# Kernel tuning notes

Hardware: AMD Instinct MI355X
Metric: run time of the kernel (lower is better)

## Reference

```python
import jax, jax.numpy as jnp
import numpy as np

NUM_HEADS = 12
LEVEL = 16
SOFTMAX_STEP = 6.0  # spiking_softmax.step

def _if_init(shape):
    # torch lazily inits q = zeros + 0.5, acc_q = zeros
    return (jnp.full(shape, 0.5, jnp.float32), jnp.zeros(shape, jnp.float32))

def _if_step(state, x, pos_max, neg_min):
    # IFNeuron with q_threshold = 1.0, borrow = 0.0 (all t-branches collapse to q += x.detach())
    q, acc = state
    q = q + jax.lax.stop_gradient(x)
    acc = jnp.round(acc)
    pos = (q - 1.0 >= 0.0) & (acc < pos_max)
    neg = (q < 0.0) & (acc > neg_min)
    out = jnp.where(pos, 1.0, jnp.where(neg, -1.0, 0.0)).astype(jnp.float32)
    return (q - out, acc + out), out

def _forward(x, w_qkv, w_proj):
    T, B, N, C = x.shape
    H = NUM_HEADS
    D = C // H
    scale = D ** -0.5
    pos_s, neg_s = LEVEL // 2 - 1, -(LEVEL // 2)  # sym=True IF neurons
    pos_u, neg_u = LEVEL // 2 - 1, 0              # sym=False (attn_softmax_IF)

    carry = (
        _if_init((B, H, N, D)), _if_init((B, H, N, D)), _if_init((B, H, N, D)),  # q/k/v IF
        _if_init((B, H, N, N)), _if_init((B, H, N, N)),                           # attn IF, softmax IF
        _if_init((B, H, N, D)), _if_init((B, N, C)),                              # after-attn IF, proj IF
        jnp.zeros((B, H, N, N), jnp.float32), jnp.zeros((B, H, N, N), jnp.float32),  # Ssoftmax X, Y_pre
    )

    def step(carry, xs):
        xt, t = xs
        qif, kif, vif, aif, sif, oif, pif, sm_X, sm_Y = carry
        qkv = (xt @ w_qkv.T).reshape(B, N, 3, H, D).transpose(2, 0, 3, 1, 4)  # [3,B,H,N,D]
        qif, q = _if_step(qif, qkv[0], pos_s, neg_s)
        kif, k = _if_step(kif, qkv[1], pos_s, neg_s)
        vif, v = _if_step(vif, qkv[2], pos_s, neg_s)
        q_s = q * scale
        q_acc = qif[1] * scale  # acc_q * scale * q_threshold (thr=1)
        k_acc = kif[1]
        # AttentionMulti incremental-sum QK^T: q_sum@k^T + q@k_sum^T - q@k^T
        attn = (jnp.einsum('bhnd,bhmd->bhnm', q_acc, k)
                + jnp.einsum('bhnd,bhmd->bhnm', q_s, k_acc)
                - jnp.einsum('bhnd,bhmd->bhnm', q_s, k))
        aif, attn = _if_step(aif, attn, pos_s, neg_s)
        # spiking_softmax: delta of (scaled) softmax over accumulated logits
        sm_X = sm_X + attn
        Y = jax.nn.softmax(sm_X, axis=-1) * jnp.minimum(t / SOFTMAX_STEP, 1.0)
        attn = Y - sm_Y
        sm_Y = Y
        sif, attn = _if_step(sif, attn, pos_u, neg_u)
        # AttentionMulti1 incremental-sum attn@V: a_sum@v + a@v_sum - a@v
        out = (jnp.einsum('bhnm,bhmd->bhnd', sif[1], v)
               + jnp.einsum('bhnm,bhmd->bhnd', attn, vif[1])
               - jnp.einsum('bhnm,bhmd->bhnd', attn, v))
        oif, out = _if_step(oif, out, pos_s, neg_s)
        out = out.transpose(0, 2, 1, 3).reshape(B, N, C) @ w_proj.T
        pif, out = _if_step(pif, out, pos_s, neg_s)
        return (qif, kif, vif, aif, sif, oif, pif, sm_X, sm_Y), out

    ts = jnp.arange(1, T + 1, dtype=jnp.float32)
    _, ys = jax.lax.scan(step, carry, (x, ts))
    return ys  # [T, B, N, C] spike outputs per timestep

def setup_inputs():
    key = jax.random.key(0)
    k1, k2, k3 = jax.random.split(key, 3)
    T, B, N, C = 8, 8, 512, 768
    x = jax.random.normal(k1, (T, B, N, C), jnp.float32)
    w_qkv = jax.random.normal(k2, (3 * C, C), jnp.float32) / np.sqrt(C)
    w_proj = jax.random.normal(k3, (C, C), jnp.float32) / np.sqrt(C)
    return {"x": x, "w_qkv": w_qkv, "w_proj": w_proj}

def reference(x, w_qkv, w_proj):
    return _forward(x, w_qkv, w_proj)
```

## Files before the change

### kernel.cpp

```cpp
#include <hip/hip_runtime.h>
#include <stdint.h>

typedef __attribute__((ext_vector_type(4))) float f32x4;
typedef __attribute__((ext_vector_type(8))) short s16x8;
typedef __attribute__((ext_vector_type(8))) char  s8x8;
typedef __attribute__((ext_vector_type(16))) char s8x16;
typedef unsigned short u16;

constexpr int    Tn  = 8;
constexpr int    Nn  = 512;
constexpr int    Cn  = 768;
constexpr int    Dn  = 64;
constexpr int    BHn = 96;
constexpr int    BNn = 4096;
constexpr int    C3n = 2304;
constexpr size_t BHND = 3145728;
constexpr size_t BHNN = 25165824;
constexpr size_t BNC  = 3145728;

__device__ float  g_qkvt8[(size_t)Tn * BNn * C3n];
__device__ int8_t g_A1[(size_t)Tn * BHND * 2];
__device__ int8_t g_B1[(size_t)Tn * BHND * 2];
__device__ short  g_S16[(size_t)Tn * BHNN];
__device__ int8_t g_v8 [(size_t)Tn * BHND];
__device__ int8_t g_vd8[(size_t)Tn * BHND];
__device__ int8_t g_vT[(size_t)Tn * BHn * Dn * 1024];
__device__ int8_t g_sifa8[(size_t)Tn * BHNN];
__device__ int8_t g_spk8[(size_t)Tn * BHNN];
__device__ short  g_pv16[(size_t)Tn * BHND];
__device__ float  g_osp8[(size_t)Tn * BNC];
__device__ float  g_proj8[(size_t)Tn * BNC];

static __device__ __forceinline__ u16 f2bf(float f) {
    union { float f; unsigned int u; } v; v.f = f;
    return (u16)(v.u >> 16);
}

static __device__ __forceinline__ s16x8 cvt_i8_bf16x8(const int8_t* p) {
    s8x8 v = *(const s8x8*)p;
    s16x8 r;
#pragma unroll
    for (int j = 0; j < 8; ++j) r[j] = (short)f2bf((float)v[j]);
    return r;
}

static __device__ __forceinline__ float if_sym(float x, float& q, int& a) {
    float q2 = q + x;
    bool pos = ((q2 - 1.0f) >= 0.0f) && (a < 7);
    bool neg = (q2 < 0.0f) && (a > -8);
    float out = pos ? 1.0f : (neg ? -1.0f : 0.0f);
    q = q2 - out;
    a += (int)out;
    return out;
}

__global__ __launch_bounds__(256) void gemm_qkv_big(
    const float* __restrict__ A, const float* __restrict__ B)
{
    __shared__ __align__(16) float As[16][132];
    __shared__ __align__(16) float Bs[16][100];
    const int tid = threadIdx.x;
    const int m0 = blockIdx.y * 128;
    const int j0 = blockIdx.x * 96;
    const int ty = tid >> 4, tx = tid & 15;

    float acc[8][6];
#pragma unroll
    for (int i = 0; i < 8; ++i)
#pragma unroll
        for (int j = 0; j < 6; ++j) acc[i][j] = 0.0f;

    for (int k0 = 0; k0 < Cn; k0 += 16) {
#pragma unroll
        for (int u = 0; u < 2; ++u) {
            int f = tid + u * 256;
            int row = f >> 2;
            int c4 = (f & 3) * 4;
            float4 av = *(const float4*)(A + (size_t)(m0 + row) * Cn + k0 + c4);
            As[c4 + 0][row] = av.x; As[c4 + 1][row] = av.y;
            As[c4 + 2][row] = av.z; As[c4 + 3][row] = av.w;
        }
#pragma unroll
        for (int u = 0; u < 3; ++u) {
            int f = tid + u * 256;
            int row = f >> 3;
            int c2 = (f & 7) * 2;
            float2 bv = *(const float2*)(B + (size_t)(j0 + row) * Cn + k0 + c2);
            Bs[c2][row] = bv.x; Bs[c2 + 1][row] = bv.y;
        }
        __syncthreads();
#pragma unroll
        for (int k = 0; k < 16; ++k) {
            alignas(16) float a[8];
            alignas(8)  float b[6];
            *(float4*)(a)     = *(const float4*)&As[k][ty * 8];
            *(float4*)(a + 4) = *(const float4*)&As[k][ty * 8 + 4];
#pragma unroll
            for (int u = 0; u < 3; ++u) {
                float2 t = *(const float2*)&Bs[k][tx * 2 + 32 * u];
                b[2 * u] = t.x; b[2 * u + 1] = t.y;
            }
#pragma unroll
            for (int i = 0; i < 8; ++i)
#pragma unroll
                for (int j = 0; j < 6; ++j)
                    acc[i][j] = fmaf(a[i], b[j], acc[i][j]);
        }
        __syncthreads();
    }
#pragma unroll
    for (int i = 0; i < 8; ++i) {
        float* cp = g_qkvt8 + (size_t)(m0 + ty * 8 + i) * C3n + j0 + tx * 2;
#pragma unroll
        for (int u = 0; u < 3; ++u) {
            float2 t; t.x = acc[i][2 * u]; t.y = acc[i][2 * u + 1];
            *(float2*)(cp + 32 * u) = t;
        }
    }
}

__global__ __launch_bounds__(256) void gemm_proj_all(const float* __restrict__ B)
{
    __shared__ __align__(16) float As[16][132];
    __shared__ __align__(16) float Bs[16][100];
    const int tid = threadIdx.x;
    const int m0 = blockIdx.y * 128;
    const int j0 = blockIdx.x * 96;
    const int ty = tid >> 4, tx = tid & 15;
    const float* A = g_osp8;

    float acc[8][6];
#pragma unroll
    for (int i = 0; i < 8; ++i)
#pragma unroll
        for (int j = 0; j < 6; ++j) acc[i][j] = 0.0f;

    for (int k0 = 0; k0 < Cn; k0 += 16) {
#pragma unroll
        for (int u = 0; u < 2; ++u) {
            int f = tid + u * 256;
            int row = f >> 2;
            int c4 = (f & 3) * 4;
            float4 av = *(const float4*)(A + (size_t)(m0 + row) * Cn + k0 + c4);
            As[c4 + 0][row] = av.x; As[c4 + 1][row] = av.y;
            As[c4 + 2][row] = av.z; As[c4 + 3][row] = av.w;
        }
#pragma unroll
        for (int u = 0; u < 3; ++u) {
            int f = tid + u * 256;
            int row = f >> 3;
            int c2 = (f & 7) * 2;
            float2 bv = *(const float2*)(B + (size_t)(j0 + row) * Cn + k0 + c2);
            Bs[c2][row] = bv.x; Bs[c2 + 1][row] = bv.y;
        }
        __syncthreads();
#pragma unroll
        for (int k = 0; k < 16; ++k) {
            alignas(16) float a[8];
            alignas(8)  float b[6];
            *(float4*)(a)     = *(const float4*)&As[k][ty * 8];
            *(float4*)(a + 4) = *(const float4*)&As[k][ty * 8 + 4];
#pragma unroll
            for (int u = 0; u < 3; ++u) {
                float2 t = *(const float2*)&Bs[k][tx * 2 + 32 * u];
                b[2 * u] = t.x; b[2 * u + 1] = t.y;
            }
#pragma unroll
            for (int i = 0; i < 8; ++i)
#pragma unroll
                for (int j = 0; j < 6; ++j)
                    acc[i][j] = fmaf(a[i], b[j], acc[i][j]);
        }
        __syncthreads();
    }
#pragma unroll
    for (int i = 0; i < 8; ++i) {
        float* cp = g_proj8 + (size_t)(m0 + ty * 8 + i) * Cn + j0 + tx * 2;
#pragma unroll
        for (int u = 0; u < 3; ++u) {
            float2 t; t.x = acc[i][2 * u]; t.y = acc[i][2 * u + 1];
            *(float2*)(cp + 32 * u) = t;
        }
    }
}

__global__ __launch_bounds__(256) void if_qkv_all() {
    int idx = blockIdx.x * 256 + threadIdx.x;
    int d = idx & 63;
    int n = (idx >> 6) & 511;
    int bh = idx >> 15;
    int b = bh / 12, h = bh - b * 12;

    float fq = 0.5f, fk = 0.5f, fv = 0.5f;
    int aq = 0, ak = 0, av = 0;

    for (int t = 0; t < Tn; ++t) {
        size_t qrow = ((size_t)((t * 8 + b) * Nn + n)) * C3n + h * 64 + d;
        float xq = g_qkvt8[qrow];
        float xk = g_qkvt8[qrow + 768];
        float xv = g_qkvt8[qrow + 1536];

        float so_q = if_sym(xq, fq, aq);
        float so_k = if_sym(xk, fk, ak);
        float so_v = if_sym(xv, fv, av);

        size_t a1b = (((size_t)t * BHn + bh) * Nn + n) * 128 + d;
        g_A1[a1b]      = (int8_t)aq;
        g_A1[a1b + 64] = (int8_t)so_q;
        g_B1[a1b]      = (int8_t)so_k;
        g_B1[a1b + 64] = (int8_t)(ak - (int)so_k);

        size_t vb = (size_t)t * BHND + (size_t)idx;
        g_v8[vb]  = (int8_t)so_v;
        g_vd8[vb] = (int8_t)(av - (int)so_v);
    }
}

__global__ __launch_bounds__(256) void vT_build() {
    int bh = blockIdx.x % BHn;
    int t  = blockIdx.x / BHn;
    const int8_t* src0 = g_v8  + (size_t)t * BHND + (size_t)bh * Nn * Dn;
    const int8_t* src1 = g_vd8 + (size_t)t * BHND + (size_t)bh * Nn * Dn;
    int8_t* dst = g_vT + ((size_t)t * BHn + bh) * Dn * 1024;
    __shared__ __align__(16) int8_t tile[64][80];
    int tid = threadIdx.x;

    for (int s = 0; s < 2; ++s) {
        const int8_t* src = s ? src1 : src0;
        int koff = s * 512;
        for (int nb = 0; nb < Nn; nb += 64) {
            {
                int n  = tid >> 2;
                int d0 = (tid & 3) * 16;
                s8x16 v = *(const s8x16*)(src + (size_t)(nb + n) * Dn + d0);
                *(s8x16*)&tile[n][d0] = v;
            }
            __syncthreads();
            {
                int d  = tid >> 2;
                int n0 = (tid & 3) * 16;
                s8x16 o;
#pragma unroll
                for (int j = 0; j < 16; ++j) o[j] = tile[n0 + j][d];
                *(s8x16*)(dst + (size_t)d * 1024 + koff + nb + n0) = o;
            }
            __syncthreads();
        }
    }
}

__global__ __launch_bounds__(256) void gemm_attn_all() {
    int t = blockIdx.z;
    int bh = blockIdx.y;
    int tm = blockIdx.x >> 3, tn = blockIdx.x & 7;
    int wave = threadIdx.x >> 6, lane = threadIdx.x & 63;
    int wr = wave >> 1, wc = wave & 1;
    int row0 = tm * 64 + wr * 32, col0 = tn * 64 + wc * 32;
    const int8_t* Ab = g_A1 + ((size_t)t * BHn + bh) * Nn * 128;
    const int8_t* Bb = g_B1 + ((size_t)t * BHn + bh) * Nn * 128;
    int lr = lane & 15, kg = (lane >> 4) * 8;
    f32x4 acc[2][2] = {};
#pragma unroll
    for (int kk = 0; kk < 128; kk += 32) {
        s16x8 a0 = cvt_i8_bf16x8(Ab + (size_t)(row0 + lr) * 128 + kk + kg);
        s16x8 a1 = cvt_i8_bf16x8(Ab + (size_t)(row0 + 16 + lr) * 128 + kk + kg);
        s16x8 b0 = cvt_i8_bf16x8(Bb + (size_t)(col0 + lr) * 128 + kk + kg);
        s16x8 b1 = cvt_i8_bf16x8(Bb + (size_t)(col0 + 16 + lr) * 128 + kk + kg);
        acc[0][0] = __builtin_amdgcn_mfma_f32_16x16x32_bf16(a0, b0, acc[0][0], 0, 0, 0);
        acc[0][1] = __builtin_amdgcn_mfma_f32_16x16x32_bf16(a0, b1, acc[0][1], 0, 0, 0);
        acc[1][0] = __builtin_amdgcn_mfma_f32_16x16x32_bf16(a1, b0, acc[1][0], 0, 0, 0);
        acc[1][1] = __builtin_amdgcn_mfma_f32_16x16x32_bf16(a1, b1, acc[1][1], 0, 0, 0);
    }
    short* Sb = g_S16 + (size_t)t * BHNN + (size_t)bh * Nn * Nn;
#pragma unroll
    for (int i = 0; i < 2; ++i)
#pragma unroll
        for (int j = 0; j < 2; ++j)
#pragma unroll
            for (int q = 0; q < 4; ++q) {
                int row = row0 + i * 16 + (lane >> 4) * 4 + q;
                int col = col0 + j * 16 + lr;
                Sb[row * Nn + col] = (short)(int)acc[i][j][q];
            }
}

__global__ __launch_bounds__(256) void attn_pipeline_all() {
    int rowid = blockIdx.x;
    size_t base = (size_t)rowid * Nn;
    int tid = threadIdx.x;
    __shared__ int   redI[4];
    __shared__ float redF[4];

    int   aq8[2]  = {4, 4};
    int   aac[2]  = {0, 0};
    float sq[2]   = {0.5f, 0.5f};
    int   sa[2]   = {0, 0};
    float yold[2] = {0.0f, 0.0f};

    for (int t = 0; t < Tn; ++t) {
        float st = (t + 1) < 6 ? (float)(t + 1) / 6.0f : 1.0f;
        const short* S = g_S16 + (size_t)t * BHNN;

        int X[2];
        int myMax = -128;
#pragma unroll
        for (int u = 0; u < 2; ++u) {
            int c = tid + u * 256;
            int s  = S[base + c];
            int q8 = aq8[u] + s;
            int a  = aac[u];
            bool pos = (q8 >= 8) && (a < 7);
            bool neg = (q8 < 0) && (a > -8);
            int o = pos ? 1 : (neg ? -1 : 0);
            aq8[u] = q8 - (o << 3);
            a += o;
            aac[u] = a;
            X[u] = a;
            myMax = max(myMax, a);
        }
        for (int off = 32; off; off >>= 1) myMax = max(myMax, __shfl_xor(myMax, off));
        if ((tid & 63) == 0) redI[tid >> 6] = myMax;
        __syncthreads();
        int M = max(max(redI[0], redI[1]), max(redI[2], redI[3]));

        float e[2];
        float mySum = 0.0f;
#pragma unroll
        for (int u = 0; u < 2; ++u) { e[u] = expf((float)(X[u] - M)); mySum += e[u]; }
        for (int off = 32; off; off >>= 1) mySum += __shfl_xor(mySum, off);
        if ((tid & 63) == 0) redF[tid >> 6] = mySum;
        __syncthreads();
        float Ssum = (redF[0] + redF[1]) + (redF[2] + redF[3]);

#pragma unroll
        for (int u = 0; u < 2; ++u) {
            int c = tid + u * 256;
            float y = (e[u] / Ssum) * st;
            float dlt = y - yold[u];
            yold[u] = y;
            float q = sq[u] + dlt;
            int a = sa[u];
            bool pos = ((q - 1.0f) >= 0.0f) && (a < 7);
            bool neg = (q < 0.0f) && (a > 0);
            float o = pos ? 1.0f : (neg ? -1.0f : 0.0f);
            sq[u] = q - o;
            a += (int)o;
            sa[u] = a;
            g_sifa8[(size_t)t * BHNN + base + c] = (int8_t)a;
            g_spk8[(size_t)t * BHNN + base + c]  = (int8_t)o;
        }
    }
}

__global__ __launch_bounds__(256) void gemm_pv_all() {
    int t = blockIdx.z;
    int bh = blockIdx.y;
    int tm = blockIdx.x;
    int wave = threadIdx.x >> 6, lane = threadIdx.x & 63;
    int wr = wave >> 1, wc = wave & 1;
    int row0 = tm * 64 + wr * 32, col0 = wc * 32;
    const int8_t* Aa  = g_sifa8 + (size_t)t * BHNN + (size_t)bh * Nn * Nn;
    const int8_t* Asp = g_spk8  + (size_t)t * BHNN + (size_t)bh * Nn * Nn;
    const int8_t* Bb  = g_vT + ((size_t)t * BHn + bh) * Dn * 1024;
    int lr = lane & 15, kg = (lane >> 4) * 8;
    f32x4 acc[2][2] = {};
    for (int kk = 0; kk < 512; kk += 32) {
        s16x8 a0 = cvt_i8_bf16x8(Aa + (size_t)(row0 + lr) * 512 + kk + kg);
        s16x8 a1 = cvt_i8_bf16x8(Aa + (size_t)(row0 + 16 + lr) * 512 + kk + kg);
        s16x8 b0 = cvt_i8_bf16x8(Bb + (size_t)(col0 + lr) * 1024 + kk + kg);
        s16x8 b1 = cvt_i8_bf16x8(Bb + (size_t)(col0 + 16 + lr) * 1024 + kk + kg);
        acc[0][0] = __builtin_amdgcn_mfma_f32_16x16x32_bf16(a0, b0, acc[0][0], 0, 0, 0);
        acc[0][1] = __builtin_amdgcn_mfma_f32_16x16x32_bf16(a0, b1, acc[0][1], 0, 0, 0);
        acc[1][0] = __builtin_amdgcn_mfma_f32_16x16x32_bf16(a1, b0, acc[1][0], 0, 0, 0);
        acc[1][1] = __builtin_amdgcn_mfma_f32_16x16x32_bf16(a1, b1, acc[1][1], 0, 0, 0);
    }
    for (int kk = 0; kk < 512; kk += 32) {
        s16x8 a0 = cvt_i8_bf16x8(Asp + (size_t)(row0 + lr) * 512 + kk + kg);
        s16x8 a1 = cvt_i8_bf16x8(Asp + (size_t)(row0 + 16 + lr) * 512 + kk + kg);
        s16x8 b0 = cvt_i8_bf16x8(Bb + (size_t)(col0 + lr) * 1024 + 512 + kk + kg);
        s16x8 b1 = cvt_i8_bf16x8(Bb + (size_t)(col0 + 16 + lr) * 1024 + 512 + kk + kg);
        acc[0][0] = __builtin_amdgcn_mfma_f32_16x16x32_bf16(a0, b0, acc[0][0], 0, 0, 0);
        acc[0][1] = __builtin_amdgcn_mfma_f32_16x16x32_bf16(a0, b1, acc[0][1], 0, 0, 0);
        acc[1][0] = __builtin_amdgcn_mfma_f32_16x16x32_bf16(a1, b0, acc[1][0], 0, 0, 0);
        acc[1][1] = __builtin_amdgcn_mfma_f32_16x16x32_bf16(a1, b1, acc[1][1], 0, 0, 0);
    }
    short* Pb = g_pv16 + (size_t)t * BHND + (size_t)bh * Nn * Dn;
#pragma unroll
    for (int i = 0; i < 2; ++i)
#pragma unroll
        for (int j = 0; j < 2; ++j)
#pragma unroll
            for (int q = 0; q < 4; ++q) {
                int row = row0 + i * 16 + (lane >> 4) * 4 + q;
                int col = col0 + j * 16 + lr;
                Pb[row * Dn + col] = (short)(int)acc[i][j][q];
            }
}

__global__ __launch_bounds__(256) void oif_all() {
    int idx = blockIdx.x * 256 + threadIdx.x;
    int d = idx & 63;
    int n = (idx >> 6) & 511;
    int bh = idx >> 15;
    int b = bh / 12, h = bh - b * 12;
    size_t obase = ((size_t)(b * Nn + n)) * Cn + h * 64 + d;

    float q = 0.5f; int a = 0;
    for (int t = 0; t < Tn; ++t) {
        float x = (float)g_pv16[(size_t)t * BHND + idx];
        float o = if_sym(x, q, a);
        g_osp8[(size_t)t * BNC + obase] = o;
    }
}

__global__ __launch_bounds__(256) void pif_all(float* __restrict__ outp) {
    int idx = blockIdx.x * 256 + threadIdx.x;
    float q = 0.5f; int a = 0;
    for (int t = 0; t < Tn; ++t) {
        float x = g_proj8[(size_t)t * BNC + idx];
        float o = if_sym(x, q, a);
        outp[(size_t)t * BNC + idx] = o;
    }
}

extern "C" void kernel_launch(void* const* d_in, const int* in_sizes, int n_in,
                              void* d_out, int out_size, void* d_ws, size_t ws_size,
                              hipStream_t stream) {
    (void)in_sizes; (void)n_in; (void)out_size; (void)d_ws; (void)ws_size;
    const float* x      = (const float*)d_in[0];
    const float* w_qkv  = (const float*)d_in[1];
    const float* w_proj = (const float*)d_in[2];
    float* outp = (float*)d_out;

    gemm_qkv_big<<<dim3(C3n / 96, (Tn * BNn) / 128), 256, 0, stream>>>(x, w_qkv);
    if_qkv_all<<<(int)(BHND / 256), 256, 0, stream>>>();
    vT_build<<<Tn * BHn, 256, 0, stream>>>();
    gemm_attn_all<<<dim3(64, BHn, Tn), 256, 0, stream>>>();
    attn_pipeline_all<<<BHn * Nn, 256, 0, stream>>>();
    gemm_pv_all<<<dim3(8, BHn, Tn), 256, 0, stream>>>();
    oif_all<<<(int)(BHND / 256), 256, 0, stream>>>();
    gemm_proj_all<<<dim3(Cn / 96, (Tn * BNn) / 128), 256, 0, stream>>>(w_proj);
    pif_all<<<(int)(BNC / 256), 256, 0, stream>>>(outp);
}
```

Before: 3.143 ms.

## Fuse IF neurons into QKV and projection GEMM epilogues via time-major row remap

```diff
diff --git a/kernel.cpp b/kernel.cpp
--- a/kernel.cpp
+++ b/kernel.cpp
@@ -18,7 +18,6 @@
 constexpr size_t BHNN = 25165824;
 constexpr size_t BNC  = 3145728;
 
-__device__ float  g_qkvt8[(size_t)Tn * BNn * C3n];
 __device__ int8_t g_A1[(size_t)Tn * BHND * 2];
 __device__ int8_t g_B1[(size_t)Tn * BHND * 2];
 __device__ short  g_S16[(size_t)Tn * BHNN];
@@ -28,8 +27,7 @@
 __device__ int8_t g_sifa8[(size_t)Tn * BHNN];
 __device__ int8_t g_spk8[(size_t)Tn * BHNN];
 __device__ short  g_pv16[(size_t)Tn * BHND];
-__device__ float  g_osp8[(size_t)Tn * BNC];
-__device__ float  g_proj8[(size_t)Tn * BNC];
+__device__ int8_t g_osp8i[(size_t)BNn * Tn * Cn];
 
 static __device__ __forceinline__ u16 f2bf(float f) {
     union { float f; unsigned int u; } v; v.f = f;
@@ -42,6 +40,10 @@
 #pragma unroll
     for (int j = 0; j < 8; ++j) r[j] = (short)f2bf((float)v[j]);
     return r;
+}
+
+static __device__ __forceinline__ void st2i8(int8_t* p, int v0, int v1) {
+    *(short*)p = (short)((v0 & 0xff) | (v1 << 8));
 }
 
 static __device__ __forceinline__ float if_sym(float x, float& q, int& a) {
@@ -54,8 +56,8 @@
     return out;
 }
 
-__global__ __launch_bounds__(256) void gemm_qkv_big(
-    const float* __restrict__ A, const float* __restrict__ B)
+__global__ __launch_bounds__(256) void gemm_qkv_fused(
+    const float* __restrict__ X, const float* __restrict__ B)
 {
     __shared__ __align__(16) float As[16][132];
     __shared__ __align__(16) float Bs[16][100];
@@ -76,7 +78,11 @@
             int f = tid + u * 256;
             int row = f >> 2;
             int c4 = (f & 3) * 4;
-            float4 av = *(const float4*)(A + (size_t)(m0 + row) * Cn + k0 + c4);
+            int m = m0 + row;
+            int t = m & 7, bn = m >> 3;
+            int b = bn >> 9, n = bn & 511;
+            const float* xr = X + ((size_t)((t * 8 + b) * Nn + n)) * Cn;
+            float4 av = *(const float4*)(xr + k0 + c4);
             As[c4 + 0][row] = av.x; As[c4 + 1][row] = av.y;
             As[c4 + 2][row] = av.z; As[c4 + 3][row] = av.w;
         }
@@ -108,111 +114,36 @@
         }
         __syncthreads();
     }
-#pragma unroll
-    for (int i = 0; i < 8; ++i) {
-        float* cp = g_qkvt8 + (size_t)(m0 + ty * 8 + i) * C3n + j0 + tx * 2;
-#pragma unroll
-        for (int u = 0; u < 3; ++u) {
-            float2 t; t.x = acc[i][2 * u]; t.y = acc[i][2 * u + 1];
-            *(float2*)(cp + 32 * u) = t;
-        }
-    }
-}
-
-__global__ __launch_bounds__(256) void gemm_proj_all(const float* __restrict__ B)
-{
-    __shared__ __align__(16) float As[16][132];
-    __shared__ __align__(16) float Bs[16][100];
-    const int tid = threadIdx.x;
-    const int m0 = blockIdx.y * 128;
-    const int j0 = blockIdx.x * 96;
-    const int ty = tid >> 4, tx = tid & 15;
-    const float* A = g_osp8;
-
-    float acc[8][6];
-#pragma unroll
-    for (int i = 0; i < 8; ++i)
-#pragma unroll
-        for (int j = 0; j < 6; ++j) acc[i][j] = 0.0f;
-
-    for (int k0 = 0; k0 < Cn; k0 += 16) {
-#pragma unroll
-        for (int u = 0; u < 2; ++u) {
-            int f = tid + u * 256;
-            int row = f >> 2;
-            int c4 = (f & 3) * 4;
-            float4 av = *(const float4*)(A + (size_t)(m0 + row) * Cn + k0 + c4);
-            As[c4 + 0][row] = av.x; As[c4 + 1][row] = av.y;
-            As[c4 + 2][row] = av.z; As[c4 + 3][row] = av.w;
-        }
-#pragma unroll
-        for (int u = 0; u < 3; ++u) {
-            int f = tid + u * 256;
-            int row = f >> 3;
-            int c2 = (f & 7) * 2;
-            float2 bv = *(const float2*)(B + (size_t)(j0 + row) * Cn + k0 + c2);
-            Bs[c2][row] = bv.x; Bs[c2 + 1][row] = bv.y;
-        }
-        __syncthreads();
-#pragma unroll
-        for (int k = 0; k < 16; ++k) {
-            alignas(16) float a[8];
-            alignas(8)  float b[6];
-            *(float4*)(a)     = *(const float4*)&As[k][ty * 8];
-            *(float4*)(a + 4) = *(const float4*)&As[k][ty * 8 + 4];
-#pragma unroll
-            for (int u = 0; u < 3; ++u) {
-                float2 t = *(const float2*)&Bs[k][tx * 2 + 32 * u];
-                b[2 * u] = t.x; b[2 * u + 1] = t.y;
-            }
-#pragma unroll
-            for (int i = 0; i < 8; ++i)
-#pragma unroll
-                for (int j = 0; j < 6; ++j)
-                    acc[i][j] = fmaf(a[i], b[j], acc[i][j]);
-        }
-        __syncthreads();
-    }
-#pragma unroll
-    for (int i = 0; i < 8; ++i) {
-        float* cp = g_proj8 + (size_t)(m0 + ty * 8 + i) * Cn + j0 + tx * 2;
-#pragma unroll
-        for (int u = 0; u < 3; ++u) {
-            float2 t; t.x = acc[i][2 * u]; t.y = acc[i][2 * u + 1];
-            *(float2*)(cp + 32 * u) = t;
-        }
-    }
-}
-
-__global__ __launch_bounds__(256) void if_qkv_all() {
-    int idx = blockIdx.x * 256 + threadIdx.x;
-    int d = idx & 63;
-    int n = (idx >> 6) & 511;
-    int bh = idx >> 15;
-    int b = bh / 12, h = bh - b * 12;
-
-    float fq = 0.5f, fk = 0.5f, fv = 0.5f;
-    int aq = 0, ak = 0, av = 0;
-
-    for (int t = 0; t < Tn; ++t) {
-        size_t qrow = ((size_t)((t * 8 + b) * Nn + n)) * C3n + h * 64 + d;
-        float xq = g_qkvt8[qrow];
-        float xk = g_qkvt8[qrow + 768];
-        float xv = g_qkvt8[qrow + 1536];
-
-        float so_q = if_sym(xq, fq, aq);
-        float so_k = if_sym(xk, fk, ak);
-        float so_v = if_sym(xv, fv, av);
-
-        size_t a1b = (((size_t)t * BHn + bh) * Nn + n) * 128 + d;
-        g_A1[a1b]      = (int8_t)aq;
-        g_A1[a1b + 64] = (int8_t)so_q;
-        g_B1[a1b]      = (int8_t)so_k;
-        g_B1[a1b + 64] = (int8_t)(ak - (int)so_k);
-
-        size_t vb = (size_t)t * BHND + (size_t)idx;
-        g_v8[vb]  = (int8_t)so_v;
-        g_vd8[vb] = (int8_t)(av - (int)so_v);
+
+    const int type = (j0 >= 1536) ? 2 : ((j0 >= 768) ? 1 : 0);
+    const int bn = (m0 + ty * 8) >> 3;
+    const int b = bn >> 9, n = bn & 511;
+#pragma unroll
+    for (int u = 0; u < 3; ++u) {
+        int c  = j0 + 32 * u + tx * 2;
+        int cl = c - type * 768;
+        int h = cl >> 6, d = cl & 63;
+        int bh = b * 12 + h;
+        float q0 = 0.5f, q1 = 0.5f;
+        int   a0 = 0,    a1 = 0;
+#pragma unroll
+        for (int t = 0; t < Tn; ++t) {
+            float o0 = if_sym(acc[t][2 * u],     q0, a0);
+            float o1 = if_sym(acc[t][2 * u + 1], q1, a1);
+            if (type == 0) {
+                size_t p = (((size_t)t * BHn + bh) * Nn + n) * 128 + d;
+                st2i8(&g_A1[p],      a0,      a1);
+                st2i8(&g_A1[p + 64], (int)o0, (int)o1);
+            } else if (type == 1) {
+                size_t p = (((size_t)t * BHn + bh) * Nn + n) * 128 + d;
+                st2i8(&g_B1[p],      (int)o0,        (int)o1);
+                st2i8(&g_B1[p + 64], a0 - (int)o0,   a1 - (int)o1);
+            } else {
+                size_t p = (size_t)t * BHND + ((size_t)bh * Nn + n) * 64 + d;
+                st2i8(&g_v8[p],  (int)o0,      (int)o1);
+                st2i8(&g_vd8[p], a0 - (int)o0, a1 - (int)o1);
+            }
+        }
     }
 }
 
@@ -403,23 +334,83 @@
     int n = (idx >> 6) & 511;
     int bh = idx >> 15;
     int b = bh / 12, h = bh - b * 12;
-    size_t obase = ((size_t)(b * Nn + n)) * Cn + h * 64 + d;
+    size_t bn = (size_t)(b * Nn + n);
+    int c = h * 64 + d;
 
     float q = 0.5f; int a = 0;
     for (int t = 0; t < Tn; ++t) {
         float x = (float)g_pv16[(size_t)t * BHND + idx];
         float o = if_sym(x, q, a);
-        g_osp8[(size_t)t * BNC + obase] = o;
-    }
-}
-
-__global__ __launch_bounds__(256) void pif_all(float* __restrict__ outp) {
-    int idx = blockIdx.x * 256 + threadIdx.x;
-    float q = 0.5f; int a = 0;
-    for (int t = 0; t < Tn; ++t) {
-        float x = g_proj8[(size_t)t * BNC + idx];
-        float o = if_sym(x, q, a);
-        outp[(size_t)t * BNC + idx] = o;
+        g_osp8i[(bn * 8 + t) * Cn + c] = (int8_t)o;
+    }
+}
+
+__global__ __launch_bounds__(256) void gemm_proj_pif_all(
+    const float* __restrict__ B, float* __restrict__ outp)
+{
+    __shared__ __align__(16) float As[16][132];
+    __shared__ __align__(16) float Bs[16][100];
+    const int tid = threadIdx.x;
+    const int m0 = blockIdx.y * 128;
+    const int j0 = blockIdx.x * 96;
+    const int ty = tid >> 4, tx = tid & 15;
+
+    float acc[8][6];
+#pragma unroll
+    for (int i = 0; i < 8; ++i)
+#pragma unroll
+        for (int j = 0; j < 6; ++j) acc[i][j] = 0.0f;
+
+    for (int k0 = 0; k0 < Cn; k0 += 16) {
+        {
+            int row = tid >> 1;
+            int c8 = (tid & 1) * 8;
+            s8x8 v = *(const s8x8*)(g_osp8i + (size_t)(m0 + row) * Cn + k0 + c8);
+#pragma unroll
+            for (int j = 0; j < 8; ++j) As[c8 + j][row] = (float)v[j];
+        }
+#pragma unroll
+        for (int u = 0; u < 3; ++u) {
+            int f = tid + u * 256;
+            int r2 = f >> 3;
+            int c2 = (f & 7) * 2;
+            float2 bv = *(const float2*)(B + (size_t)(j0 + r2) * Cn + k0 + c2);
+            Bs[c2][r2] = bv.x; Bs[c2 + 1][r2] = bv.y;
+        }
+        __syncthreads();
+#pragma unroll
+        for (int k = 0; k < 16; ++k) {
+            alignas(16) float a[8];
+            alignas(8)  float b[6];
+            *(float4*)(a)     = *(const float4*)&As[k][ty * 8];
+            *(float4*)(a + 4) = *(const float4*)&As[k][ty * 8 + 4];
+#pragma unroll
+            for (int u = 0; u < 3; ++u) {
+                float2 t = *(const float2*)&Bs[k][tx * 2 + 32 * u];
+                b[2 * u] = t.x; b[2 * u + 1] = t.y;
+            }
+#pragma unroll
+            for (int i = 0; i < 8; ++i)
+#pragma unroll
+                for (int j = 0; j < 6; ++j)
+                    acc[i][j] = fmaf(a[i], b[j], acc[i][j]);
+        }
+        __syncthreads();
+    }
+
+    const size_t bn = (size_t)((m0 + ty * 8) >> 3);
+#pragma unroll
+    for (int u = 0; u < 3; ++u) {
+        size_t cbase = bn * Cn + j0 + 32 * u + tx * 2;
+        float q0 = 0.5f, q1 = 0.5f;
+        int   a0 = 0,    a1 = 0;
+#pragma unroll
+        for (int t = 0; t < Tn; ++t) {
+            float o0 = if_sym(acc[t][2 * u],     q0, a0);
+            float o1 = if_sym(acc[t][2 * u + 1], q1, a1);
+            float2 st; st.x = o0; st.y = o1;
+            *(float2*)(outp + (size_t)t * BNC + cbase) = st;
+        }
     }
 }
 
@@ -432,13 +423,11 @@
     const float* w_proj = (const float*)d_in[2];
     float* outp = (float*)d_out;
 
-    gemm_qkv_big<<<dim3(C3n / 96, (Tn * BNn) / 128), 256, 0, stream>>>(x, w_qkv);
-    if_qkv_all<<<(int)(BHND / 256), 256, 0, stream>>>();
+    gemm_qkv_fused<<<dim3(C3n / 96, (Tn * BNn) / 128), 256, 0, stream>>>(x, w_qkv);
     vT_build<<<Tn * BHn, 256, 0, stream>>>();
     gemm_attn_all<<<dim3(64, BHn, Tn), 256, 0, stream>>>();
     attn_pipeline_all<<<BHn * Nn, 256, 0, stream>>>();
     gemm_pv_all<<<dim3(8, BHn, Tn), 256, 0, stream>>>();
     oif_all<<<(int)(BHND / 256), 256, 0, stream>>>();
-    gemm_proj_all<<<dim3(Cn / 96, (Tn * BNn) / 128), 256, 0, stream>>>(w_proj);
-    pif_all<<<(int)(BNC / 256), 256, 0, stream>>>(outp);
-}
+    gemm_proj_pif_all<<<dim3(Cn / 96, (Tn * BNn) / 128), 256, 0, stream>>>(w_proj, outp);
+}
```

Measured after the change: 2.994 ms. 1.05x faster.
